# Optimization experiments

Measured on AMD Instinct MI355X. Metric: run time of the kernel, lower is better.

## Reference

```python
import jax, jax.numpy as jnp
import numpy as np

B, SE, HE, DE = 32, 256, 512, 2
HD = DE * HE            # decoder hidden (h0 reshape implies Hd = De*He)
ED = 256                # label embedding dim
N = 8192                # seq label num (output_size)
T = 20                  # decode_max_seq_len (eval path)
KE = VE = 1024
MD = 256
EIN = ED + HE           # LSTM input size
EOS_ID = 0
SPARCE_RATE = 0.8
NEG = -1.0e7
MAXV = 1.0e9
EPS = 1e-8


def setup_inputs() -> dict:
    key = jax.random.key(0)
    ks = jax.random.split(key, 20)
    s = 0.05
    return {
        'encoded_hidden_embeddings': jax.random.normal(ks[0], (B, SE, HE), jnp.float32),
        'hidden': jax.random.normal(ks[1], (DE, B, HE), jnp.float32),
        'cell': jax.random.normal(ks[2], (DE, B, HE), jnp.float32),
        'text_lengths': jax.random.randint(ks[3], (B,), 1, SE + 1),
        'encoder_mask': jnp.ones((B, SE), bool),
        'memory_key_mask': jnp.ones((B, KE), bool),
        'memory_key_embedding': jax.random.normal(ks[4], (B, KE, MD), jnp.float32),
        'memory_value_mask': jnp.ones((B, VE), bool),
        'memory_value_embedding': jax.random.normal(ks[5], (B, VE, MD), jnp.float32),
        # parameters
        'W_ih': jax.random.normal(ks[6], (4 * HD, EIN), jnp.float32) * s,
        'W_hh': jax.random.normal(ks[7], (4 * HD, HD), jnp.float32) * s,
        'b_ih': jnp.zeros((4 * HD,), jnp.float32),
        'b_hh': jnp.zeros((4 * HD,), jnp.float32),
        'mlp_W1': jax.random.normal(ks[8], (HD, HD), jnp.float32) * s,
        'mlp_b1': jnp.zeros((HD,), jnp.float32),
        'mlp_W2': jax.random.normal(ks[9], (N, HD), jnp.float32) * s,
        'mlp_b2': jnp.zeros((N,), jnp.float32),
        'emb_table': jax.random.normal(ks[10], (N, ED), jnp.float32) * s,
        'dense_W': jax.random.normal(ks[11], (HE, ED), jnp.float32) * s,
        'dense_b': jnp.zeros((HE,), jnp.float32),
        'read_W': jax.random.normal(ks[12], (MD, EIN), jnp.float32) * s,
        'read_b': jnp.zeros((MD,), jnp.float32),
    }


def _cos(a, b):
    num = jnp.sum(a * b, axis=-1)
    den = jnp.maximum(jnp.linalg.norm(a, axis=-1) * jnp.linalg.norm(b, axis=-1), EPS)
    return num / den


def _lstm(x, h, c, W_ih, W_hh, b_ih, b_hh):
    g = x @ W_ih.T + b_ih + h @ W_hh.T + b_hh
    i, f, gg, o = jnp.split(g, 4, axis=-1)  # torch gate order i,f,g,o
    c1 = jax.nn.sigmoid(f) * c + jax.nn.sigmoid(i) * jnp.tanh(gg)
    h1 = jax.nn.sigmoid(o) * jnp.tanh(c1)
    return h1, c1


def _forward(enc, hidden, cell, encoder_mask, memory_key_mask, memory_value_mask,
             mem_k, mem_v, W_ih, W_hh, b_ih, b_hh, mlp_W1, mlp_b1, mlp_W2, mlp_b2,
             emb_table, dense_W, dense_b, read_W, read_b):
    h0 = jnp.transpose(hidden, (1, 0, 2)).reshape(B, HD)
    c0 = jnp.transpose(cell, (1, 0, 2)).reshape(B, HD)
    pad = jnp.where(encoder_mask, 0.0, -MAXV).astype(enc.dtype)  # (B,Se)
    sent = enc[:, 0, :]                                           # (B,He)
    x0 = jnp.zeros((B, EIN), enc.dtype)
    mask0 = jnp.zeros((B, N), enc.dtype)

    def step(carry, _):
        h, c, x, lmask = carry
        h, c = _lstm(x, h, c, W_ih, W_hh, b_ih, b_hh)
        hid = jax.nn.relu(h @ mlp_W1.T + mlp_b1)
        logits = hid @ mlp_W2.T + mlp_b2 + lmask          # (B,N)
        nid = jnp.argmax(logits, axis=-1)                 # (B,) greedy decode
        lab = emb_table[nid]                              # (B,Ed)
        lmask = lmask.at[jnp.arange(B), nid].set(NEG)     # scatter-mask used ids
        lmask = lmask.at[:, EOS_ID].set(0.0)              # EOS always allowed
        q = lab @ dense_W.T + dense_b                     # (B,He)
        score = jnp.einsum('bse,be->bs', enc, q) + pad
        w = jax.nn.softmax(score, axis=-1)
        attn = jnp.einsum('bse,bs->be', enc, w)
        x = jnp.concatenate([lab, sent + attn], axis=-1)  # (B,Ed+He)
        mq = x @ read_W.T + read_b                        # (B,Md)
        ksim = _cos(mq[:, None, :], mem_k)                # (B,Ke)
        return (h, c, x, lmask), (logits, nid, ksim)

    _, (outputs, next_ids, key_sims) = jax.lax.scan(step, (h0, c0, x0, mask0), None, length=T)
    outputs = jnp.transpose(outputs, (1, 0, 2))           # (B,T,N)
    next_ids = next_ids.T                                 # (B,T)
    key_sims = jnp.transpose(key_sims, (1, 0, 2))         # (B,T,Ke)

    key_sim = jnp.max(key_sims, axis=1)                   # (B,Ke)
    key_sim = jnp.where(key_sim < 0, 0.0, key_sim)
    # mapping_weight: pairwise cosine between memory keys and values (B,Ke,Ve)
    mw = _cos(mem_k[:, :, None, :], mem_v[:, None, :, :])
    keep = (mw >= jnp.max(mw, axis=-1, keepdims=True)) & (mw >= SPARCE_RATE)
    mw = jnp.where(keep, mw, 0.0)
    val_sim = jnp.einsum('bk,bkv->bv', key_sim, mw)       # (B,Ve)
    key_out = jnp.where(memory_key_mask, key_sim, -1.0)
    val_out = jnp.where(memory_value_mask, val_sim, -1.0)
    return outputs, next_ids, key_out, val_out


def reference(encoded_hidden_embeddings, hidden, cell, text_lengths, encoder_mask,
              memory_key_mask, memory_key_embedding, memory_value_mask, memory_value_embedding,
              W_ih, W_hh, b_ih, b_hh, mlp_W1, mlp_b1, mlp_W2, mlp_b2,
              emb_table, dense_W, dense_b, read_W, read_b):
    del text_lengths  # unused in module math
    return _forward(encoded_hidden_embeddings, hidden, cell, encoder_mask,
                    memory_key_mask, memory_value_mask, memory_key_embedding,
                    memory_value_embedding, W_ih, W_hh, b_ih, b_hh,
                    mlp_W1, mlp_b1, mlp_W2, mlp_b2, emb_table,
                    dense_W, dense_b, read_W, read_b)
```

## Files before the change

kernel.cpp:

```cpp
#include <hip/hip_runtime.h>
#include <cstdint>
#include <cstddef>

#define B_   32
#define SE_  256
#define HE_  512
#define HD_  1024
#define ED_  256
#define N_   8192
#define T_   20
#define KE_  1024
#define VE_  1024
#define MD_  256
#define EIN_ 768
#define NEG_   (-10000000.0f)
#define MAXV_  (1000000000.0f)
#define EPS_   (1e-8f)
#define SPARSE_ 0.8f
#define GATE_  0.78f

#define NLOGB (N_/16)

#define O_IDS  (B_*T_*N_)
#define O_KEY  (O_IDS + B_*T_)
#define O_VAL  (O_KEY + B_*KE_)

typedef __attribute__((ext_vector_type(8))) short short8;
typedef __attribute__((ext_vector_type(4))) float floatx4;

__device__ __forceinline__ float sigf(float v) { return 1.0f / (1.0f + expf(-v)); }

__device__ __forceinline__ short f2bf(float f) {
    union { float f; unsigned u; } v; v.f = f;
    unsigned r = v.u + 0x7FFFu + ((v.u >> 16) & 1u);
    return (short)(r >> 16);
// ... 122 lines not shown
                int byt = (vrow * 512 + kc * 64 + lq * 16) ^ ((vrow & 7) << 4);
                bfr[kc] = *(const short8*)((char*)Vs + byt);
            }
            #pragma unroll
            for (int rg = 0; rg < 2; ++rg) {
                floatx4 acc = {0.0f, 0.0f, 0.0f, 0.0f};
                #pragma unroll
                for (int kc = 0; kc < 8; ++kc)
                    acc = __builtin_amdgcn_mfma_f32_16x16x32_bf16(af[rg][kc], bfr[kc], acc, 0, 0, 0);
                #pragma unroll
                for (int reg = 0; reg < 4; ++reg) {
                    float cs = acc[reg] / fmaxf(nk[rg][reg] * nv, EPS_);
                    rmax[rg][reg] = fmaxf(rmax[rg][reg], cs);
                }
            }
        }
    }
    #pragma unroll
    for (int rg = 0; rg < 2; ++rg)
        #pragma unroll
        for (int reg = 0; reg < 4; ++reg) {
            float v = rmax[rg][reg];
            v = fmaxf(v, __shfl_xor(v, 1, 64));
            v = fmaxf(v, __shfl_xor(v, 2, 64));
            v = fmaxf(v, __shfl_xor(v, 4, 64));
            v = fmaxf(v, __shfl_xor(v, 8, 64));
            if (lrow == 0) {
                int* p = (int*)&rowmax[(size_t)b * KE_ + rowbase + rg * 16 + lq * 4 + reg];
                atomicMax(p, __float_as_int(fmaxf(v, 0.0f)));
            }
        }
}


__global__ __launch_bounds__(256) void k_gates(
    const float* __restrict__ x, const float* __restrict__ W_ih,
    const float* __restrict__ h_in, const float* __restrict__ W_hh,
    const float* __restrict__ b_ih, const float* __restrict__ b_hh,
    float* __restrict__ c_st, float* __restrict__ h_out)
{
    __shared__ __align__(16) float Xs[32 * 256];
    __shared__ float red[16][32][17];
    const int tid = threadIdx.x;
    const int kg = tid & 15, jg = (tid >> 4) & 3, bg = tid >> 6;
    const int ch0 = blockIdx.x * 4;

    float acc[4][8];
    #pragma unroll
    for (int jv = 0; jv < 4; ++jv)
        #pragma unroll
        for (int bv = 0; bv < 8; ++bv) acc[jv][bv] = 0.0f;

    for (int k0 = 0; k0 < EIN_ + HD_; k0 += 256) {
        const bool second = (k0 >= EIN_);
        const float* Xsrc = second ? h_in : x;
        const float* Wsrc = second ? W_hh : W_ih;
        const int srcK = second ? HD_ : EIN_;
        const int ks = second ? (k0 - EIN_) : k0;
        __syncthreads();
        #pragma unroll
        for (int i = 0; i < 8; ++i) {
            int lin = tid + i * 256;
            int bb = lin >> 6, q = lin & 63;
            *(float4*)&Xs[bb * 256 + q * 4] = *(const float4*)(Xsrc + (size_t)bb * srcK + ks + q * 4);
        }
        __syncthreads();
// ... 79 lines not shown
            for (int bv = 0; bv < 8; ++bv) {
                float4 x4 = *(const float4*)&Xs[(bg * 8 + bv) * 256 + qc * 4];
                #pragma unroll
                for (int jv = 0; jv < 4; ++jv) {
                    acc[jv][bv] = fmaf(wv[jv].x, x4.x, acc[jv][bv]);
                    acc[jv][bv] = fmaf(wv[jv].y, x4.y, acc[jv][bv]);
                    acc[jv][bv] = fmaf(wv[jv].z, x4.z, acc[jv][bv]);
                    acc[jv][bv] = fmaf(wv[jv].w, x4.w, acc[jv][bv]);
                }
            }
        }
    }
    #pragma unroll
    for (int jv = 0; jv < 4; ++jv)
        #pragma unroll
        for (int bv = 0; bv < 8; ++bv)
            red[jg * 4 + jv][bg * 8 + bv][kg] = acc[jv][bv];
    __syncthreads();
    for (int o = tid; o < 16 * B_; o += 256) {
        int jjo = o >> 5, b = o & 31;
        float s = 0.0f;
        #pragma unroll
        for (int k = 0; k < 16; ++k) s += red[jjo][b][k];
        int jo = jbase + jjo;
        s += bias[jo];
        if (relu) s = fmaxf(s, 0.0f);
        out[(size_t)b * outStride + jo] = s;
    }
}

__global__ __launch_bounds__(256) void k_logits(
    const float* __restrict__ hid, const float* __restrict__ W2,
    const float* __restrict__ b2, const float* __restrict__ lmask,
    float* __restrict__ lg_out ,
    float* __restrict__ pval, int* __restrict__ pidx)
{
    __shared__ __align__(16) float Xs[32 * 256];
    __shared__ float red[16][32][17];
    const int tid = threadIdx.x;
    const int kg = tid & 15, jg = (tid >> 4) & 3, bg = tid >> 6;
    const int jbase = blockIdx.x * 16;

    float acc[4][8];
    #pragma unroll
    for (int jv = 0; jv < 4; ++jv)
        #pragma unroll
        for (int bv = 0; bv < 8; ++bv) acc[jv][bv] = 0.0f;

    for (int k0 = 0; k0 < HD_; k0 += 256) {
        __syncthreads();
        #pragma unroll
        for (int i = 0; i < 8; ++i) {
            int lin = tid + i * 256;
            int bb = lin >> 6, q = lin & 63;
            *(float4*)&Xs[bb * 256 + q * 4] = *(const float4*)(hid + (size_t)bb * HD_ + k0 + q * 4);
        }
        __syncthreads();
        #pragma unroll
        for (int qq = 0; qq < 4; ++qq) {
            const int qc = kg + qq * 16;
            float4 wv[4];
            #pragma unroll
            for (int jv = 0; jv < 4; ++jv)
                wv[jv] = *(const float4*)(W2 + (size_t)(jbase + jg * 4 + jv) * HD_ + k0 + qc * 4);
            #pragma unroll
            for (int bv = 0; bv < 8; ++bv) {
                float4 x4 = *(const float4*)&Xs[(bg * 8 + bv) * 256 + qc * 4];
                #pragma unroll
// ... 6 lines not shown
            }
        }
    }
    #pragma unroll
    for (int jv = 0; jv < 4; ++jv)
        #pragma unroll
        for (int bv = 0; bv < 8; ++bv)
            red[jg * 4 + jv][bg * 8 + bv][kg] = acc[jv][bv];
    __syncthreads();
    for (int o = tid; o < 16 * B_; o += 256) {
        int jjo = o >> 5, b = o & 31;
        float s = 0.0f;
        #pragma unroll
        for (int k = 0; k < 16; ++k) s += red[jjo][b][k];
        int jo = jbase + jjo;
        s += b2[jo] + lmask[(size_t)b * N_ + jo];
        lg_out[(size_t)b * (T_ * N_) + jo] = s;
        red[jjo][b][16] = s;
    }
    __syncthreads();
    if (tid < 32) {
        int b = tid;
        float best = -1e38f; int bi = 0;
        #pragma unroll
        for (int jjo = 0; jjo < 16; ++jjo) {
            float v = red[jjo][b][16];
            if (v > best) { best = v; bi = jjo; }
        }
        pval[(size_t)b * NLOGB + blockIdx.x] = best;
        pidx[(size_t)b * NLOGB + blockIdx.x] = jbase + bi;
    }
}

__global__ __launch_bounds__(256) void k_merge(
    const float* __restrict__ pval, const int* __restrict__ pidx,
    float* __restrict__ d_out, int t, int* __restrict__ nidbuf,
    float* __restrict__ lmask, const float* __restrict__ emb,
    const float* __restrict__ dense_W, const float* __restrict__ dense_b,
    float* __restrict__ qbuf)
{
    __shared__ float sv[256];
    __shared__ int   si[256];
    __shared__ __align__(16) float lab[ED_];
    const int b = blockIdx.x, tid = threadIdx.x;
    float best = -1e38f; int bi = N_;
    for (int p = tid; p < NLOGB; p += 256) {
        float v = pval[(size_t)b * NLOGB + p];
        int   i = pidx[(size_t)b * NLOGB + p];
        if (v > best || (v == best && i < bi)) { best = v; bi = i; }
    }
    sv[tid] = best; si[tid] = bi;
    __syncthreads();
    for (int s = 128; s > 0; s >>= 1) {
        if (tid < s) {
            float v2 = sv[tid + s]; int i2 = si[tid + s];
            if (v2 > sv[tid] || (v2 == sv[tid] && i2 < si[tid])) { sv[tid] = v2; si[tid] = i2; }
        }
        __syncthreads();
    }
    int nid = si[0];
    if (tid == 0) {
        nidbuf[b] = nid;
        d_out[O_IDS + (size_t)b * T_ + t] = (float)nid;
        lmask[(size_t)b * N_ + nid] = NEG_;
        lmask[(size_t)b * N_] = 0.0f;
    }
    lab[tid] = emb[(size_t)nid * ED_ + tid];
    __syncthreads();
    const float4* Lq = (const float4*)lab;
    #pragma unroll
    for (int jj = 0; jj < 2; ++jj) {
        int j = tid + jj * 256;
        const float4* Wq = (const float4*)(dense_W + (size_t)j * ED_);
        float s0 = 0.0f, s1 = 0.0f, s2 = 0.0f, s3 = 0.0f;
        #pragma unroll
        for (int q = 0; q < 64; q += 4) {
            float4 w0 = Wq[q],   x0 = Lq[q];
            float4 w1 = Wq[q+1], x1 = Lq[q+1];
            float4 w2 = Wq[q+2], x2 = Lq[q+2];
            float4 w3 = Wq[q+3], x3 = Lq[q+3];
            s0 = fmaf(w0.x,x0.x,s0); s0 = fmaf(w0.y,x0.y,s0); s0 = fmaf(w0.z,x0.z,s0); s0 = fmaf(w0.w,x0.w,s0);
            s1 = fmaf(w1.x,x1.x,s1); s1 = fmaf(w1.y,x1.y,s1); s1 = fmaf(w1.z,x1.z,s1); s1 = fmaf(w1.w,x1.w,s1);
            s2 = fmaf(w2.x,x2.x,s2); s2 = fmaf(w2.y,x2.y,s2); s2 = fmaf(w2.z,x2.z,s2); s2 = fmaf(w2.w,x2.w,s2);
            s3 = fmaf(w3.x,x3.x,s3); s3 = fmaf(w3.y,x3.y,s3); s3 = fmaf(w3.z,x3.z,s3); s3 = fmaf(w3.w,x3.w,s3);
        }
        qbuf[(size_t)b * HE_ + j] = dense_b[j] + ((s0 + s1) + (s2 + s3));
    }
}

__device__ __forceinline__ float wave_dot(const float* __restrict__ row, const float* vl, int quads)
{
    int lane = threadIdx.x & 63;
    float s = 0.0f;
    for (int q = lane; q < quads; q += 64) {
        float4 a = ((const float4*)row)[q];
        float4 x = ((const float4*)vl)[q];
        s = fmaf(a.x, x.x, s); s = fmaf(a.y, x.y, s);
        s = fmaf(a.z, x.z, s); s = fmaf(a.w, x.w, s);
    }
    for (int m = 32; m; m >>= 1) s += __shfl_xor(s, m, 64);
    return s;
}

__global__ __launch_bounds__(256) void k_attn1(
    const float* __restrict__ qg, const float* __restrict__ enc,
    const float* __restrict__ pad, float* __restrict__ part)
{
    __shared__ __align__(16) float ql[HE_];
    __shared__ float sc_l[32];
    __shared__ float wp_l[32];
    const int b = blockIdx.y, sc = blockIdx.x;
    const int tid = threadIdx.x, lane = tid & 63, w = tid >> 6;
    ql[tid] = qg[(size_t)b * HE_ + tid];
    ql[tid + 256] = qg[(size_t)b * HE_ + tid + 256];
    __syncthreads();

    #pragma unroll
    for (int i = 0; i < 8; ++i) {
        int sl = w + i * 4;
        int s = sc * 32 + sl;
        float v = wave_dot(enc + ((size_t)b * SE_ + s) * HE_, ql, HE_ / 4);
        if (lane == 0) sc_l[sl] = v + pad[b * SE_ + s];
    }
    __syncthreads();

    float m = -1e38f;
    #pragma unroll
    for (int i = 0; i < 32; ++i) m = fmaxf(m, sc_l[i]);
    if (tid < 32) wp_l[tid] = expf(sc_l[tid] - m);
    __syncthreads();
    float esum = 0.0f;
    #pragma unroll
    for (int i = 0; i < 32; ++i) esum += wp_l[i];

    float a0 = 0.0f, a1 = 0.0f;
    for (int i = 0; i < 32; ++i) {
        float wv = wp_l[i];
        const float* er = enc + ((size_t)b * SE_ + sc * 32 + i) * HE_;
        a0 = fmaf(wv, er[tid], a0);
        a1 = fmaf(wv, er[tid + 256], a1);
    }
    float* pb = part + ((size_t)b * 8 + sc) * 516;
    pb[tid] = a0;
    pb[256 + tid] = a1;
    if (tid == 0) { pb[512] = m; pb[513] = esum; }
}

__global__ __launch_bounds__(256) void k_attn2read(
    const float* __restrict__ part, const float* __restrict__ sent,
    const int* __restrict__ nidbuf, const float* __restrict__ emb,
    const float* __restrict__ read_W, const float* __restrict__ read_b,
    float* __restrict__ xg, float* __restrict__ mqg)
{
    __shared__ float ms[8], es[8];
    __shared__ __align__(16) float xl[EIN_];
    const int qv = blockIdx.x, b = blockIdx.y;
    const int tid = threadIdx.x;
    if (tid < 8) {
        ms[tid] = part[((size_t)b * 8 + tid) * 516 + 512];
        es[tid] = part[((size_t)b * 8 + tid) * 516 + 513];
    }
    __syncthreads();
    float m = -1e38f;
    #pragma unroll
    for (int c = 0; c < 8; ++c) m = fmaxf(m, ms[c]);
    float scale[8];
    float denom = 0.0f;
    #pragma unroll
    for (int c = 0; c < 8; ++c) { scale[c] = expf(ms[c] - m); denom += es[c] * scale[c]; }
    float inv = 1.0f / denom;
    float a0 = 0.0f, a1 = 0.0f;
    #pragma unroll
    for (int c = 0; c < 8; ++c) {
        const float* pb = part + ((size_t)b * 8 + c) * 516;
        a0 = fmaf(scale[c], pb[tid], a0);
        a1 = fmaf(scale[c], pb[256 + tid], a1);
    }
    a0 *= inv; a1 *= inv;
    int nid = nidbuf[b];
    xl[tid]             = emb[(size_t)nid * ED_ + tid];
    xl[ED_ + tid]       = sent[(size_t)b * HE_ + tid]       + a0;
    xl[ED_ + 256 + tid] = sent[(size_t)b * HE_ + 256 + tid] + a1;
    __syncthreads();
    if (qv == 0) {
        float* xr = xg + (size_t)b * EIN_;
        xr[tid] = xl[tid]; xr[tid + 256] = xl[tid + 256]; xr[tid + 512] = xl[tid + 512];
    }
    const int r = qv * 64 + (tid >> 2), kq = tid & 3;
    const float4* Wq = (const float4*)(read_W + (size_t)r * EIN_ + kq * 192);
    const float4* xq = (const float4*)(xl + kq * 192);
    float s0 = 0.0f, s1 = 0.0f, s2 = 0.0f, s3 = 0.0f;
    #pragma unroll
    for (int q = 0; q < 48; q += 4) {
        float4 w0 = Wq[q],   v0 = xq[q];
        float4 w1 = Wq[q+1], v1 = xq[q+1];
        float4 w2 = Wq[q+2], v2 = xq[q+2];
        float4 w3 = Wq[q+3], v3 = xq[q+3];
        s0 = fmaf(w0.x,v0.x,s0); s0 = fmaf(w0.y,v0.y,s0); s0 = fmaf(w0.z,v0.z,s0); s0 = fmaf(w0.w,v0.w,s0);
        s1 = fmaf(w1.x,v1.x,s1); s1 = fmaf(w1.y,v1.y,s1); s1 = fmaf(w1.z,v1.z,s1); s1 = fmaf(w1.w,v1.w,s1);
        s2 = fmaf(w2.x,v2.x,s2); s2 = fmaf(w2.y,v2.y,s2); s2 = fmaf(w2.z,v2.z,s2); s2 = fmaf(w2.w,v2.w,s2);
        s3 = fmaf(w3.x,v3.x,s3); s3 = fmaf(w3.y,v3.y,s3); s3 = fmaf(w3.w,v3.w,s3); s3 = fmaf(w3.z,v3.z,s3);
    }
    float s = ((s0 + s1) + (s2 + s3));
    s += __shfl_xor(s, 1, 64);
    s += __shfl_xor(s, 2, 64);
    if (kq == 0) mqg[(size_t)b * MD_ + r] = s + read_b[r];
}

__global__ __launch_bounds__(256) void k_ksim(
    const float* __restrict__ mqg,
    const float* __restrict__ mem_k, const float* __restrict__ normk,
    float* __restrict__ key_run)
{
    __shared__ __align__(16) float mql[MD_];
    __shared__ float red[256];
    const int b = blockIdx.y, kt = blockIdx.x;
    const int tid = threadIdx.x, lane = tid & 63, w = tid >> 6;
    float mv = mqg[(size_t)b * MD_ + tid];
    mql[tid] = mv;
    red[tid] = mv * mv;
    __syncthreads();
    for (int s = 128; s > 0; s >>= 1) { if (tid < s) red[tid] += red[tid + s]; __syncthreads(); }
    float nmq = sqrtf(red[0]);

    int base = kt * 64 + w * 16;
    for (int i = 0; i < 16; ++i) {
        int k = base + i;
        float num = wave_dot(mem_k + ((size_t)b * KE_ + k) * MD_, mql, MD_ / 4);
        if (lane == 0) {
            float cs = num / fmaxf(nmq * normk[b * KE_ + k], EPS_);
            float o = key_run[b * KE_ + k];
            key_run[b * KE_ + k] = fmaxf(o, cs);
        }
    }
}

__global__ __launch_bounds__(256) void k_keyfinal(
    float* __restrict__ key_run, const void* __restrict__ kmask, float* __restrict__ d_out)
{
    int idx = blockIdx.x * 256 + threadIdx.x;
    bool b8 = mask_is_b8(kmask);
    float v = key_run[idx];
    v = (v < 0.0f) ? 0.0f : v;
    key_run[idx] = v;
    d_out[O_KEY + idx] = mask_at(kmask, idx, b8) ? v : -1.0f;
}

__global__ __launch_bounds__(256) void k_val(
    const float* __restrict__ rowmax, const float* __restrict__ mem_k, const float* __restrict__ mem_v,
    const float* __restrict__ normk, const float* __restrict__ normv,
    const float* __restrict__ key_sim, float* __restrict__ val_sim)
{
    int idx = blockIdx.x * 256 + threadIdx.x;
// ... 40 lines not shown
    const float* mem_k    = (const float*)d_in[6];
    const void*  vmask    = d_in[7];
    const float* mem_v    = (const float*)d_in[8];
    const float* W_ih     = (const float*)d_in[9];
    const float* W_hh     = (const float*)d_in[10];
    const float* b_ih     = (const float*)d_in[11];
    const float* b_hh     = (const float*)d_in[12];
    const float* mlp_W1   = (const float*)d_in[13];
    const float* mlp_b1   = (const float*)d_in[14];
    const float* mlp_W2   = (const float*)d_in[15];
    const float* mlp_b2   = (const float*)d_in[16];
    const float* emb      = (const float*)d_in[17];
    const float* dense_W  = (const float*)d_in[18];
    const float* dense_b  = (const float*)d_in[19];
    const float* read_W   = (const float*)d_in[20];
    const float* read_b   = (const float*)d_in[21];
    float* d_out = (float*)d_out_v;
    float* ws = (float*)d_ws;

    float* hA      = ws;
    float* hB      = ws + 32768;
    float* c       = ws + 65536;
    float* x       = ws + 98304;
    float* hid     = ws + 122880;
    float* lmask   = ws + 155648;
    float* sent    = ws + 417792;
    float* pad     = ws + 434176;
    float* key_run = ws + 442368;
    float* val_sim = ws + 475136;
    float* normk   = ws + 507904;
    float* normv   = ws + 540672;
    float* rowmax  = ws + 573440;
    int*   nidbuf  = (int*)(ws + 606208);
    float* mqg     = ws + 606272;
    float* qbuf    = ws + 614464;
    float* part    = ws + 630848;
    float* pval    = ws + 762944;
    int*   pidx    = (int*)(ws + 779328);

    k_init<<<1024, 256, 0, stream>>>(hidden, cell, enc, encmask, hA, c, x, lmask, sent, pad, key_run, val_sim, rowmax);
    k_norms<<<256, 256, 0, stream>>>(mem_k, mem_v, normk, normv);
    k_rowmax_mfma<<<dim3(8, 4, 32), 256, 0, stream>>>(mem_k, mem_v, normk, normv, rowmax);

    const float* hin = hA;
    float* hout = hB;
    for (int t = 0; t < T_; ++t) {
        k_gates<<<256, 256, 0, stream>>>(x, W_ih, hin, W_hh, b_ih, b_hh, c, hout);
        k_gemm3<<<HD_ / 16, 256, 0, stream>>>(hout, mlp_W1, HD_, mlp_b1, hid, HD_, 1);
        k_logits<<<N_ / 16, 256, 0, stream>>>(hid, mlp_W2, mlp_b2, lmask,
                                              d_out + (size_t)t * N_, pval, pidx);
        k_merge<<<B_, 256, 0, stream>>>(pval, pidx, d_out, t, nidbuf, lmask,
                                        emb, dense_W, dense_b, qbuf);
        k_attn1<<<dim3(8, B_), 256, 0, stream>>>(qbuf, enc, pad, part);
        k_attn2read<<<dim3(4, B_), 256, 0, stream>>>(part, sent, nidbuf, emb, read_W, read_b, x, mqg);
        k_ksim<<<dim3(16, B_), 256, 0, stream>>>(mqg, mem_k, normk, key_run);
        float* tmp = (float*)hin; hin = hout; hout = tmp;
    }

    k_keyfinal<<<128, 256, 0, stream>>>(key_run, kmask, d_out);
    k_val<<<128, 256, 0, stream>>>(rowmax, mem_k, mem_v, normk, normv, key_run, val_sim);
    k_valout<<<128, 256, 0, stream>>>(val_sim, vmask, d_out);
}
```

Measured before the change: 2.900 ms.

## Fuse per-step decoder kernels into one cooperative persistent kernel with grid syncs

Replaces the seven per-timestep kernel launches (140 total) with a single cooperative kernel that loops over timesteps and separates the stages with grid.sync(). The goal is to remove launch overhead and inter-kernel gaps in a latency-bound decode loop. Work per stage is spread over the grid with block-stride loops. The grid is capped at 512 blocks, so the gates and logits stages run with less parallelism than before, and grid-wide barriers carry their own cost. If the cooperative launch is unavailable, the code falls back to the old launch sequence.

```diff
diff --git a/kernel.cpp b/kernel.cpp
--- a/kernel.cpp
+++ b/kernel.cpp
@@ -1,6 +1,9 @@
 #include <hip/hip_runtime.h>
+#include <hip/hip_cooperative_groups.h>
 #include <cstdint>
 #include <cstddef>
+
+namespace cg = cooperative_groups;
 
 #define B_   32
 #define SE_  256
@@ -189,6 +192,397 @@
         }
 }
 
+__device__ __forceinline__ float wave_dot(const float* __restrict__ row, const float* vl, int quads)
+{
+    int lane = threadIdx.x & 63;
+    float s = 0.0f;
+    for (int q = lane; q < quads; q += 64) {
+        float4 a = ((const float4*)row)[q];
+        float4 x = ((const float4*)vl)[q];
+        s = fmaf(a.x, x.x, s); s = fmaf(a.y, x.y, s);
+        s = fmaf(a.z, x.z, s); s = fmaf(a.w, x.w, s);
+    }
+    for (int m = 32; m; m >>= 1) s += __shfl_xor(s, m, 64);
+    return s;
+}
+
+struct MegaArgs {
+    const float *enc, *pad, *sent;
+    const float *W_ih, *W_hh, *b_ih, *b_hh;
+    const float *mlp_W1, *mlp_b1, *mlp_W2, *mlp_b2;
+    const float *emb, *dense_W, *dense_b, *read_W, *read_b;
+    const float *mem_k, *normk;
+    float *hA, *hB, *c, *x, *hid, *lmask, *key_run, *d_out;
+    float *qbuf, *mqg, *part, *pval;
+    int *nidbuf, *pidx;
+};
+
+template<int JV>
+__device__ __forceinline__ void gemm_core(
+    const float* __restrict__ X, int K, const float* __restrict__ W, int jbase,
+    float* Xs, float (*g_red)[33], int tid)
+{
+    const int kg = tid & 15, jg = (tid >> 4) & 3, bg = tid >> 6;
+    float acc[JV][8];
+    #pragma unroll
+    for (int jv = 0; jv < JV; ++jv)
+        #pragma unroll
+        for (int bv = 0; bv < 8; ++bv) acc[jv][bv] = 0.0f;
+
+    for (int k0 = 0; k0 < K; k0 += 256) {
+        __syncthreads();
+        #pragma unroll
+        for (int i = 0; i < 8; ++i) {
+            int lin = tid + i * 256;
+            int bb = lin >> 6, q = lin & 63;
+            *(float4*)&Xs[bb * 256 + q * 4] = *(const float4*)(X + (size_t)bb * K + k0 + q * 4);
+        }
+        __syncthreads();
+        #pragma unroll
+        for (int qq = 0; qq < 4; ++qq) {
+            const int qc = kg + qq * 16;
+            float4 wv[JV];
+            #pragma unroll
+            for (int jv = 0; jv < JV; ++jv)
+                wv[jv] = *(const float4*)(W + (size_t)(jbase + jg * JV + jv) * K + k0 + qc * 4);
+            #pragma unroll
+            for (int bv = 0; bv < 8; ++bv) {
+                float4 x4 = *(const float4*)&Xs[(bg * 8 + bv) * 256 + qc * 4];
+                #pragma unroll
+                for (int jv = 0; jv < JV; ++jv) {
+                    acc[jv][bv] = fmaf(wv[jv].x, x4.x, acc[jv][bv]);
+                    acc[jv][bv] = fmaf(wv[jv].y, x4.y, acc[jv][bv]);
+                    acc[jv][bv] = fmaf(wv[jv].z, x4.z, acc[jv][bv]);
+                    acc[jv][bv] = fmaf(wv[jv].w, x4.w, acc[jv][bv]);
+                }
+            }
+        }
+    }
+    #pragma unroll
+    for (int jv = 0; jv < JV; ++jv)
+        #pragma unroll
+        for (int bv = 0; bv < 8; ++bv) {
+            float v = acc[jv][bv];
+            v += __shfl_xor(v, 1, 64);
+            v += __shfl_xor(v, 2, 64);
+            v += __shfl_xor(v, 4, 64);
+            v += __shfl_xor(v, 8, 64);
+            acc[jv][bv] = v;
+        }
+    __syncthreads();
+    if (kg == 0) {
+        #pragma unroll
+        for (int jv = 0; jv < JV; ++jv)
+            #pragma unroll
+            for (int bv = 0; bv < 8; ++bv)
+                g_red[jg * JV + jv][bg * 8 + bv] = acc[jv][bv];
+    }
+    __syncthreads();
+}
+
+__global__ __launch_bounds__(256) void k_megaloop(MegaArgs a)
+{
+    cg::grid_group grid = cg::this_grid();
+    __shared__ __align__(16) float Xs[32 * 256];
+    __shared__ float g_red[16][33];
+    const int tid = threadIdx.x, lane = tid & 63, w = tid >> 6;
+
+    for (int t = 0; t < T_; ++t) {
+        const float* hin  = (t & 1) ? a.hB : a.hA;
+        float*       hout = (t & 1) ? a.hA : a.hB;
+
+        for (int u = blockIdx.x; u < 512; u += gridDim.x) {
+            const int kg = tid & 15, jg = (tid >> 4) & 3, bg = tid >> 6;
+            const int ch0 = u * 2;
+            float acc[2][8];
+            #pragma unroll
+            for (int jv = 0; jv < 2; ++jv)
+                #pragma unroll
+                for (int bv = 0; bv < 8; ++bv) acc[jv][bv] = 0.0f;
+
+            for (int k0 = 0; k0 < EIN_ + HD_; k0 += 256) {
+                const bool second = (k0 >= EIN_);
+                const float* Xsrc = second ? hin : a.x;
+                const float* Wsrc = second ? a.W_hh : a.W_ih;
+                const int srcK = second ? HD_ : EIN_;
+                const int ks = second ? (k0 - EIN_) : k0;
+                __syncthreads();
+                #pragma unroll
+                for (int i = 0; i < 8; ++i) {
+                    int lin = tid + i * 256;
+                    int bb = lin >> 6, q = lin & 63;
+                    *(float4*)&Xs[bb * 256 + q * 4] = *(const float4*)(Xsrc + (size_t)bb * srcK + ks + q * 4);
+                }
+                __syncthreads();
+                #pragma unroll
+                for (int qq = 0; qq < 4; ++qq) {
+                    const int qc = kg + qq * 16;
+                    float4 wv[2];
+                    #pragma unroll
+                    for (int jv = 0; jv < 2; ++jv)
+                        wv[jv] = *(const float4*)(Wsrc + (size_t)(jg * HD_ + ch0 + jv) * srcK + ks + qc * 4);
+                    #pragma unroll
+                    for (int bv = 0; bv < 8; ++bv) {
+                        float4 x4 = *(const float4*)&Xs[(bg * 8 + bv) * 256 + qc * 4];
+                        #pragma unroll
+                        for (int jv = 0; jv < 2; ++jv) {
+                            acc[jv][bv] = fmaf(wv[jv].x, x4.x, acc[jv][bv]);
+                            acc[jv][bv] = fmaf(wv[jv].y, x4.y, acc[jv][bv]);
+                            acc[jv][bv] = fmaf(wv[jv].z, x4.z, acc[jv][bv]);
+                            acc[jv][bv] = fmaf(wv[jv].w, x4.w, acc[jv][bv]);
+                        }
+                    }
+                }
+            }
+            #pragma unroll
+            for (int jv = 0; jv < 2; ++jv)
+                #pragma unroll
+                for (int bv = 0; bv < 8; ++bv) {
+                    float v = acc[jv][bv];
+                    v += __shfl_xor(v, 1, 64);
+                    v += __shfl_xor(v, 2, 64);
+                    v += __shfl_xor(v, 4, 64);
+                    v += __shfl_xor(v, 8, 64);
+                    acc[jv][bv] = v;
+                }
+            __syncthreads();
+            if (kg == 0) {
+                #pragma unroll
+                for (int jv = 0; jv < 2; ++jv)
+                    #pragma unroll
+                    for (int bv = 0; bv < 8; ++bv)
+                        g_red[jg * 2 + jv][bg * 8 + bv] = acc[jv][bv];
+            }
+            __syncthreads();
+            if (tid < 64) {
+                const int c2 = tid >> 5, b = tid & 31;
+                float g4[4];
+                #pragma unroll
+                for (int gate = 0; gate < 4; ++gate) {
+                    int row = gate * HD_ + ch0 + c2;
+                    g4[gate] = g_red[gate * 2 + c2][b] + a.b_ih[row] + a.b_hh[row];
+                }
+                int idx = b * HD_ + ch0 + c2;
+                float c1 = sigf(g4[1]) * a.c[idx] + sigf(g4[0]) * tanhf(g4[2]);
+                hout[idx] = sigf(g4[3]) * tanhf(c1);
+                a.c[idx] = c1;
+            }
+        }
+        grid.sync();
+
+        for (int u = blockIdx.x; u < 256; u += gridDim.x) {
+            gemm_core<1>(hout, HD_, a.mlp_W1, u * 4, Xs, g_red, tid);
+            if (tid < 128) {
+                int jjo = tid >> 5, b = tid & 31;
+                int jo = u * 4 + jjo;
+                a.hid[(size_t)b * HD_ + jo] = fmaxf(g_red[jjo][b] + a.mlp_b1[jo], 0.0f);
+            }
+        }
+        grid.sync();
+
+        for (int u = blockIdx.x; u < 512; u += gridDim.x) {
+            gemm_core<4>(a.hid, HD_, a.mlp_W2, u * 16, Xs, g_red, tid);
+            for (int o = tid; o < 512; o += 256) {
+                int jjo = o >> 5, b = o & 31;
+                int jo = u * 16 + jjo;
+                float s = g_red[jjo][b] + a.mlp_b2[jo] + a.lmask[(size_t)b * N_ + jo];
+                a.d_out[(size_t)b * (T_ * N_) + (size_t)t * N_ + jo] = s;
+                g_red[jjo][b] = s;
+            }
+            __syncthreads();
+            if (tid < 32) {
+                int b = tid;
+                float best = -1e38f; int bi = 0;
+                #pragma unroll
+                for (int jjo = 0; jjo < 16; ++jjo) {
+                    float v = g_red[jjo][b];
+                    if (v > best) { best = v; bi = jjo; }
+                }
+                a.pval[(size_t)b * NLOGB + u] = best;
+                a.pidx[(size_t)b * NLOGB + u] = u * 16 + bi;
+            }
+            __syncthreads();
+        }
+        grid.sync();
+
+        for (int u = blockIdx.x; u < 32; u += gridDim.x) {
+            const int b = u;
+            float* sv = Xs;
+            int*   si = (int*)(Xs + 256);
+            float* lab = Xs + 512;
+            __syncthreads();
+            float best = -1e38f; int bi = N_;
+            for (int p = tid; p < NLOGB; p += 256) {
+                float v = a.pval[(size_t)b * NLOGB + p];
+                int   i = a.pidx[(size_t)b * NLOGB + p];
+                if (v > best || (v == best && i < bi)) { best = v; bi = i; }
+            }
+            sv[tid] = best; si[tid] = bi;
+            __syncthreads();
+            for (int s = 128; s > 0; s >>= 1) {
+                if (tid < s) {
+                    float v2 = sv[tid + s]; int i2 = si[tid + s];
+                    if (v2 > sv[tid] || (v2 == sv[tid] && i2 < si[tid])) { sv[tid] = v2; si[tid] = i2; }
+                }
+                __syncthreads();
+            }
+            int nid = si[0];
+            if (tid == 0) {
+                a.nidbuf[b] = nid;
+                a.d_out[O_IDS + (size_t)b * T_ + t] = (float)nid;
+                a.lmask[(size_t)b * N_ + nid] = NEG_;
+                a.lmask[(size_t)b * N_] = 0.0f;
+            }
+            lab[tid] = a.emb[(size_t)nid * ED_ + tid];
+            __syncthreads();
+            const float4* Lq = (const float4*)lab;
+            #pragma unroll
+            for (int jj = 0; jj < 2; ++jj) {
+                int j = tid + jj * 256;
+                const float4* Wq = (const float4*)(a.dense_W + (size_t)j * ED_);
+                float s0 = 0.0f, s1 = 0.0f, s2 = 0.0f, s3 = 0.0f;
+                #pragma unroll
+                for (int q = 0; q < 64; q += 4) {
+                    float4 w0 = Wq[q],   x0 = Lq[q];
+                    float4 w1 = Wq[q+1], x1 = Lq[q+1];
+                    float4 w2 = Wq[q+2], x2 = Lq[q+2];
+                    float4 w3 = Wq[q+3], x3 = Lq[q+3];
+                    s0 = fmaf(w0.x,x0.x,s0); s0 = fmaf(w0.y,x0.y,s0); s0 = fmaf(w0.z,x0.z,s0); s0 = fmaf(w0.w,x0.w,s0);
+                    s1 = fmaf(w1.x,x1.x,s1); s1 = fmaf(w1.y,x1.y,s1); s1 = fmaf(w1.z,x1.z,s1); s1 = fmaf(w1.w,x1.w,s1);
+                    s2 = fmaf(w2.x,x2.x,s2); s2 = fmaf(w2.y,x2.y,s2); s2 = fmaf(w2.z,x2.z,s2); s2 = fmaf(w2.w,x2.w,s2);
+                    s3 = fmaf(w3.x,x3.x,s3); s3 = fmaf(w3.y,x3.y,s3); s3 = fmaf(w3.z,x3.z,s3); s3 = fmaf(w3.w,x3.w,s3);
+                }
+                a.qbuf[(size_t)b * HE_ + j] = a.dense_b[j] + ((s0 + s1) + (s2 + s3));
+            }
+            __syncthreads();
+        }
+        grid.sync();
+
+        for (int u = blockIdx.x; u < 256; u += gridDim.x) {
+            const int sc = u & 7, b = u >> 3;
+            float* ql = Xs;
+            float* sc_l = Xs + 512;
+            float* wp_l = Xs + 544;
+            __syncthreads();
+            ql[tid] = a.qbuf[(size_t)b * HE_ + tid];
+            ql[tid + 256] = a.qbuf[(size_t)b * HE_ + tid + 256];
+            __syncthreads();
+            #pragma unroll
+            for (int i = 0; i < 8; ++i) {
+                int sl = w + i * 4;
+                int s = sc * 32 + sl;
+                float v = wave_dot(a.enc + ((size_t)b * SE_ + s) * HE_, ql, HE_ / 4);
+                if (lane == 0) sc_l[sl] = v + a.pad[b * SE_ + s];
+            }
+            __syncthreads();
+            float m = -1e38f;
+            #pragma unroll
+            for (int i = 0; i < 32; ++i) m = fmaxf(m, sc_l[i]);
+            if (tid < 32) wp_l[tid] = expf(sc_l[tid] - m);
+            __syncthreads();
+            float esum = 0.0f;
+            #pragma unroll
+            for (int i = 0; i < 32; ++i) esum += wp_l[i];
+            float a0 = 0.0f, a1 = 0.0f;
+            for (int i = 0; i < 32; ++i) {
+                float wv = wp_l[i];
+                const float* er = a.enc + ((size_t)b * SE_ + sc * 32 + i) * HE_;
+                a0 = fmaf(wv, er[tid], a0);
+                a1 = fmaf(wv, er[tid + 256], a1);
+            }
+            float* pb = a.part + ((size_t)b * 8 + sc) * 516;
+            pb[tid] = a0;
+            pb[256 + tid] = a1;
+            if (tid == 0) { pb[512] = m; pb[513] = esum; }
+            __syncthreads();
+        }
+        grid.sync();
+
+        for (int u = blockIdx.x; u < 128; u += gridDim.x) {
+            const int qv = u & 3, b = u >> 2;
+            float* xl = Xs;
+            float* ms = Xs + 768;
+            float* es = Xs + 776;
+            __syncthreads();
+            if (tid < 8) {
+                ms[tid] = a.part[((size_t)b * 8 + tid) * 516 + 512];
+                es[tid] = a.part[((size_t)b * 8 + tid) * 516 + 513];
+            }
+            __syncthreads();
+            float m = -1e38f;
+            #pragma unroll
+            for (int c8 = 0; c8 < 8; ++c8) m = fmaxf(m, ms[c8]);
+            float scale[8];
+            float denom = 0.0f;
+            #pragma unroll
+            for (int c8 = 0; c8 < 8; ++c8) { scale[c8] = expf(ms[c8] - m); denom += es[c8] * scale[c8]; }
+            float inv = 1.0f / denom;
+            float a0 = 0.0f, a1 = 0.0f;
+            #pragma unroll
+            for (int c8 = 0; c8 < 8; ++c8) {
+                const float* pb = a.part + ((size_t)b * 8 + c8) * 516;
+                a0 = fmaf(scale[c8], pb[tid], a0);
+                a1 = fmaf(scale[c8], pb[256 + tid], a1);
+            }
+            a0 *= inv; a1 *= inv;
+            int nid = a.nidbuf[b];
+            xl[tid]             = a.emb[(size_t)nid * ED_ + tid];
+            xl[ED_ + tid]       = a.sent[(size_t)b * HE_ + tid]       + a0;
+            xl[ED_ + 256 + tid] = a.sent[(size_t)b * HE_ + 256 + tid] + a1;
+            __syncthreads();
+            if (qv == 0) {
+                float* xr = a.x + (size_t)b * EIN_;
+                xr[tid] = xl[tid]; xr[tid + 256] = xl[tid + 256]; xr[tid + 512] = xl[tid + 512];
+            }
+            const int r = qv * 64 + (tid >> 2), kq = tid & 3;
+            const float4* Wq = (const float4*)(a.read_W + (size_t)r * EIN_ + kq * 192);
+            const float4* xq = (const float4*)(xl + kq * 192);
+            float s0 = 0.0f, s1 = 0.0f, s2 = 0.0f, s3 = 0.0f;
+            #pragma unroll
+            for (int q = 0; q < 48; q += 4) {
+                float4 w0 = Wq[q],   v0 = xq[q];
+                float4 w1 = Wq[q+1], v1 = xq[q+1];
+                float4 w2 = Wq[q+2], v2 = xq[q+2];
+                float4 w3 = Wq[q+3], v3 = xq[q+3];
+                s0 = fmaf(w0.x,v0.x,s0); s0 = fmaf(w0.y,v0.y,s0); s0 = fmaf(w0.z,v0.z,s0); s0 = fmaf(w0.w,v0.w,s0);
+                s1 = fmaf(w1.x,v1.x,s1); s1 = fmaf(w1.y,v1.y,s1); s1 = fmaf(w1.z,v1.z,s1); s1 = fmaf(w1.w,v1.w,s1);
+                s2 = fmaf(w2.x,v2.x,s2); s2 = fmaf(w2.y,v2.y,s2); s2 = fmaf(w2.z,v2.z,s2); s2 = fmaf(w2.w,v2.w,s2);
+                s3 = fmaf(w3.x,v3.x,s3); s3 = fmaf(w3.y,v3.y,s3); s3 = fmaf(w3.z,v3.z,s3); s3 = fmaf(w3.w,v3.w,s3);
+            }
+            float s = ((s0 + s1) + (s2 + s3));
+            s += __shfl_xor(s, 1, 64);
+            s += __shfl_xor(s, 2, 64);
+            if (kq == 0) a.mqg[(size_t)b * MD_ + r] = s + a.read_b[r];
+            __syncthreads();
+        }
+        grid.sync();
+
+        for (int u = blockIdx.x; u < 512; u += gridDim.x) {
+            const int kt = u & 15, b = u >> 4;
+            float* mql = Xs;
+            float* red = Xs + 256;
+            __syncthreads();
+            float mv = a.mqg[(size_t)b * MD_ + tid];
+            mql[tid] = mv;
+            red[tid] = mv * mv;
+            __syncthreads();
+            for (int s = 128; s > 0; s >>= 1) { if (tid < s) red[tid] += red[tid + s]; __syncthreads(); }
+            float nmq = sqrtf(red[0]);
+            int base = kt * 64 + w * 16;
+            for (int i = 0; i < 16; ++i) {
+                int k = base + i;
+                float num = wave_dot(a.mem_k + ((size_t)b * KE_ + k) * MD_, mql, MD_ / 4);
+                if (lane == 0) {
+                    float cs = num / fmaxf(nmq * a.normk[b * KE_ + k], EPS_);
+                    float o = a.key_run[b * KE_ + k];
+                    a.key_run[b * KE_ + k] = fmaxf(o, cs);
+                }
+            }
+            __syncthreads();
+        }
+        grid.sync();
+    }
+}
 
 __global__ __launch_bounds__(256) void k_gates(
     const float* __restrict__ x, const float* __restrict__ W_ih,
@@ -334,8 +728,7 @@
 __global__ __launch_bounds__(256) void k_logits(
     const float* __restrict__ hid, const float* __restrict__ W2,
     const float* __restrict__ b2, const float* __restrict__ lmask,
-    float* __restrict__ lg_out ,
-    float* __restrict__ pval, int* __restrict__ pidx)
+    float* __restrict__ lg_out, float* __restrict__ pval, int* __restrict__ pidx)
 {
     __shared__ __align__(16) float Xs[32 * 256];
     __shared__ float red[16][32][17];
@@ -464,20 +857,6 @@
     }
 }
 
-__device__ __forceinline__ float wave_dot(const float* __restrict__ row, const float* vl, int quads)
-{
-    int lane = threadIdx.x & 63;
-    float s = 0.0f;
-    for (int q = lane; q < quads; q += 64) {
-        float4 a = ((const float4*)row)[q];
-        float4 x = ((const float4*)vl)[q];
-        s = fmaf(a.x, x.x, s); s = fmaf(a.y, x.y, s);
-        s = fmaf(a.z, x.z, s); s = fmaf(a.w, x.w, s);
-    }
-    for (int m = 32; m; m >>= 1) s += __shfl_xor(s, m, 64);
-    return s;
-}
-
 __global__ __launch_bounds__(256) void k_attn1(
     const float* __restrict__ qg, const float* __restrict__ enc,
     const float* __restrict__ pad, float* __restrict__ part)
@@ -575,7 +954,7 @@
         s0 = fmaf(w0.x,v0.x,s0); s0 = fmaf(w0.y,v0.y,s0); s0 = fmaf(w0.z,v0.z,s0); s0 = fmaf(w0.w,v0.w,s0);
         s1 = fmaf(w1.x,v1.x,s1); s1 = fmaf(w1.y,v1.y,s1); s1 = fmaf(w1.z,v1.z,s1); s1 = fmaf(w1.w,v1.w,s1);
         s2 = fmaf(w2.x,v2.x,s2); s2 = fmaf(w2.y,v2.y,s2); s2 = fmaf(w2.z,v2.z,s2); s2 = fmaf(w2.w,v2.w,s2);
-        s3 = fmaf(w3.x,v3.x,s3); s3 = fmaf(w3.y,v3.y,s3); s3 = fmaf(w3.w,v3.w,s3); s3 = fmaf(w3.z,v3.z,s3);
+        s3 = fmaf(w3.x,v3.x,s3); s3 = fmaf(w3.y,v3.y,s3); s3 = fmaf(w3.z,v3.z,s3); s3 = fmaf(w3.w,v3.w,s3);
     }
     float s = ((s0 + s1) + (s2 + s3));
     s += __shfl_xor(s, 1, 64);
@@ -711,19 +1090,49 @@
     k_norms<<<256, 256, 0, stream>>>(mem_k, mem_v, normk, normv);
     k_rowmax_mfma<<<dim3(8, 4, 32), 256, 0, stream>>>(mem_k, mem_v, normk, normv, rowmax);
 
-    const float* hin = hA;
-    float* hout = hB;
-    for (int t = 0; t < T_; ++t) {
-        k_gates<<<256, 256, 0, stream>>>(x, W_ih, hin, W_hh, b_ih, b_hh, c, hout);
-        k_gemm3<<<HD_ / 16, 256, 0, stream>>>(hout, mlp_W1, HD_, mlp_b1, hid, HD_, 1);
-        k_logits<<<N_ / 16, 256, 0, stream>>>(hid, mlp_W2, mlp_b2, lmask,
-                                              d_out + (size_t)t * N_, pval, pidx);
-        k_merge<<<B_, 256, 0, stream>>>(pval, pidx, d_out, t, nidbuf, lmask,
-                                        emb, dense_W, dense_b, qbuf);
-        k_attn1<<<dim3(8, B_), 256, 0, stream>>>(qbuf, enc, pad, part);
-        k_attn2read<<<dim3(4, B_), 256, 0, stream>>>(part, sent, nidbuf, emb, read_W, read_b, x, mqg);
-        k_ksim<<<dim3(16, B_), 256, 0, stream>>>(mqg, mem_k, normk, key_run);
-        float* tmp = (float*)hin; hin = hout; hout = tmp;
+    bool coop = true;
+    int maxb = 0;
+    if (hipOccupancyMaxActiveBlocksPerMultiprocessor(&maxb, k_megaloop, 256, 0) != hipSuccess || maxb < 1)
+        coop = false;
+    int ncu = 0;
+    if (coop) {
+        int dev = 0;
+        hipGetDevice(&dev);
+        if (hipDeviceGetAttribute(&ncu, hipDeviceAttributeMultiprocessorCount, dev) != hipSuccess || ncu < 1)
+            coop = false;
+    }
+    if (coop) {
+        int grid = maxb * ncu;
+        if (grid > 512) grid = 512;
+        MegaArgs ma;
+        ma.enc = enc; ma.pad = pad; ma.sent = sent;
+        ma.W_ih = W_ih; ma.W_hh = W_hh; ma.b_ih = b_ih; ma.b_hh = b_hh;
+        ma.mlp_W1 = mlp_W1; ma.mlp_b1 = mlp_b1; ma.mlp_W2 = mlp_W2; ma.mlp_b2 = mlp_b2;
+        ma.emb = emb; ma.dense_W = dense_W; ma.dense_b = dense_b; ma.read_W = read_W; ma.read_b = read_b;
+        ma.mem_k = mem_k; ma.normk = normk;
+        ma.hA = hA; ma.hB = hB; ma.c = c; ma.x = x; ma.hid = hid;
+        ma.lmask = lmask; ma.key_run = key_run; ma.d_out = d_out;
+        ma.qbuf = qbuf; ma.mqg = mqg; ma.part = part; ma.pval = pval;
+        ma.nidbuf = nidbuf; ma.pidx = pidx;
+        void* args[] = { (void*)&ma };
+        hipError_t le = hipLaunchCooperativeKernel(k_megaloop, dim3(grid), dim3(256), args, 0, stream);
+        if (le != hipSuccess) { (void)hipGetLastError(); coop = false; }
+    }
+    if (!coop) {
+        const float* hin = hA;
+        float* hout = hB;
+        for (int t = 0; t < T_; ++t) {
+            k_gates<<<256, 256, 0, stream>>>(x, W_ih, hin, W_hh, b_ih, b_hh, c, hout);
+            k_gemm3<<<HD_ / 16, 256, 0, stream>>>(hout, mlp_W1, HD_, mlp_b1, hid, HD_, 1);
+            k_logits<<<N_ / 16, 256, 0, stream>>>(hid, mlp_W2, mlp_b2, lmask,
+                                                  d_out + (size_t)t * N_, pval, pidx);
+            k_merge<<<B_, 256, 0, stream>>>(pval, pidx, d_out, t, nidbuf, lmask,
+                                            emb, dense_W, dense_b, qbuf);
+            k_attn1<<<dim3(8, B_), 256, 0, stream>>>(qbuf, enc, pad, part);
+            k_attn2read<<<dim3(4, B_), 256, 0, stream>>>(part, sent, nidbuf, emb, read_W, read_b, x, mqg);
+            k_ksim<<<dim3(16, B_), 256, 0, stream>>>(mqg, mem_k, normk, key_run);
+            float* tmp = (float*)hin; hin = hout; hout = tmp;
+        }
     }
 
     k_keyfinal<<<128, 256, 0, stream>>>(key_run, kmask, d_out);
```

Result: no change. 2.903 ms (+0.1%).

## Fuse merge into attention-score kernel and read projection into key-similarity kernel

Applied to the files above, without the earlier changes.

Each decode step drops from seven launches to five. The argmax merge and label dense projection are recomputed redundantly in every attention chunk block, and the memory-read projection is recomputed in every key-similarity tile block. This removes two launches per step and the qbuf and mqg global round trips. In exchange it duplicates the pval reduction and dense_W work eight times and the read_W GEMV sixteen times per batch row.

```diff
diff --git a/kernel.cpp b/kernel.cpp
--- a/kernel.cpp
+++ b/kernel.cpp
@@ -189,6 +189,19 @@
         }
 }
 
+__device__ __forceinline__ float wave_dot(const float* __restrict__ row, const float* vl, int quads)
+{
+    int lane = threadIdx.x & 63;
+    float s = 0.0f;
+    for (int q = lane; q < quads; q += 64) {
+        float4 a = ((const float4*)row)[q];
+        float4 x = ((const float4*)vl)[q];
+        s = fmaf(a.x, x.x, s); s = fmaf(a.y, x.y, s);
+        s = fmaf(a.z, x.z, s); s = fmaf(a.w, x.w, s);
+    }
+    for (int m = 32; m; m >>= 1) s += __shfl_xor(s, m, 64);
+    return s;
+}
 
 __global__ __launch_bounds__(256) void k_gates(
     const float* __restrict__ x, const float* __restrict__ W_ih,
@@ -334,8 +347,7 @@
 __global__ __launch_bounds__(256) void k_logits(
     const float* __restrict__ hid, const float* __restrict__ W2,
     const float* __restrict__ b2, const float* __restrict__ lmask,
-    float* __restrict__ lg_out ,
-    float* __restrict__ pval, int* __restrict__ pidx)
+    float* __restrict__ lg_out, float* __restrict__ pval, int* __restrict__ pidx)
 {
     __shared__ __align__(16) float Xs[32 * 256];
     __shared__ float red[16][32][17];
@@ -408,17 +420,23 @@
     }
 }
 
-__global__ __launch_bounds__(256) void k_merge(
+__global__ __launch_bounds__(256) void k_attn1m(
     const float* __restrict__ pval, const int* __restrict__ pidx,
+    const float* __restrict__ emb, const float* __restrict__ dense_W,
+    const float* __restrict__ dense_b,
+    const float* __restrict__ enc, const float* __restrict__ pad,
     float* __restrict__ d_out, int t, int* __restrict__ nidbuf,
-    float* __restrict__ lmask, const float* __restrict__ emb,
-    const float* __restrict__ dense_W, const float* __restrict__ dense_b,
-    float* __restrict__ qbuf)
+    float* __restrict__ lmask, float* __restrict__ part)
 {
     __shared__ float sv[256];
     __shared__ int   si[256];
     __shared__ __align__(16) float lab[ED_];
-    const int b = blockIdx.x, tid = threadIdx.x;
+    __shared__ __align__(16) float ql[HE_];
+    __shared__ float sc_l[32];
+    __shared__ float wp_l[32];
+    const int b = blockIdx.y, sc = blockIdx.x;
+    const int tid = threadIdx.x, lane = tid & 63, w = tid >> 6;
+
     float best = -1e38f; int bi = N_;
     for (int p = tid; p < NLOGB; p += 256) {
         float v = pval[(size_t)b * NLOGB + p];
@@ -435,7 +453,7 @@
         __syncthreads();
     }
     int nid = si[0];
-    if (tid == 0) {
+    if (sc == 0 && tid == 0) {
         nidbuf[b] = nid;
         d_out[O_IDS + (size_t)b * T_ + t] = (float)nid;
         lmask[(size_t)b * N_ + nid] = NEG_;
@@ -443,6 +461,7 @@
     }
     lab[tid] = emb[(size_t)nid * ED_ + tid];
     __syncthreads();
+
     const float4* Lq = (const float4*)lab;
     #pragma unroll
     for (int jj = 0; jj < 2; ++jj) {
@@ -460,35 +479,8 @@
             s2 = fmaf(w2.x,x2.x,s2); s2 = fmaf(w2.y,x2.y,s2); s2 = fmaf(w2.z,x2.z,s2); s2 = fmaf(w2.w,x2.w,s2);
             s3 = fmaf(w3.x,x3.x,s3); s3 = fmaf(w3.y,x3.y,s3); s3 = fmaf(w3.z,x3.z,s3); s3 = fmaf(w3.w,x3.w,s3);
         }
-        qbuf[(size_t)b * HE_ + j] = dense_b[j] + ((s0 + s1) + (s2 + s3));
-    }
-}
-
-__device__ __forceinline__ float wave_dot(const float* __restrict__ row, const float* vl, int quads)
-{
-    int lane = threadIdx.x & 63;
-    float s = 0.0f;
-    for (int q = lane; q < quads; q += 64) {
-        float4 a = ((const float4*)row)[q];
-        float4 x = ((const float4*)vl)[q];
-        s = fmaf(a.x, x.x, s); s = fmaf(a.y, x.y, s);
-        s = fmaf(a.z, x.z, s); s = fmaf(a.w, x.w, s);
-    }
-    for (int m = 32; m; m >>= 1) s += __shfl_xor(s, m, 64);
-    return s;
-}
-
-__global__ __launch_bounds__(256) void k_attn1(
-    const float* __restrict__ qg, const float* __restrict__ enc,
-    const float* __restrict__ pad, float* __restrict__ part)
-{
-    __shared__ __align__(16) float ql[HE_];
-    __shared__ float sc_l[32];
-    __shared__ float wp_l[32];
-    const int b = blockIdx.y, sc = blockIdx.x;
-    const int tid = threadIdx.x, lane = tid & 63, w = tid >> 6;
-    ql[tid] = qg[(size_t)b * HE_ + tid];
-    ql[tid + 256] = qg[(size_t)b * HE_ + tid + 256];
+        ql[j] = dense_b[j] + ((s0 + s1) + (s2 + s3));
+    }
     __syncthreads();
 
     #pragma unroll
@@ -522,16 +514,20 @@
     if (tid == 0) { pb[512] = m; pb[513] = esum; }
 }
 
-__global__ __launch_bounds__(256) void k_attn2read(
+__global__ __launch_bounds__(256) void k_attn2ksim(
     const float* __restrict__ part, const float* __restrict__ sent,
     const int* __restrict__ nidbuf, const float* __restrict__ emb,
     const float* __restrict__ read_W, const float* __restrict__ read_b,
-    float* __restrict__ xg, float* __restrict__ mqg)
+    const float* __restrict__ mem_k, const float* __restrict__ normk,
+    float* __restrict__ xg, float* __restrict__ key_run)
 {
     __shared__ float ms[8], es[8];
     __shared__ __align__(16) float xl[EIN_];
-    const int qv = blockIdx.x, b = blockIdx.y;
-    const int tid = threadIdx.x;
+    __shared__ __align__(16) float mql[MD_];
+    __shared__ float red[256];
+    const int kt = blockIdx.x, b = blockIdx.y;
+    const int tid = threadIdx.x, lane = tid & 63, w = tid >> 6;
+
     if (tid < 8) {
         ms[tid] = part[((size_t)b * 8 + tid) * 516 + 512];
         es[tid] = part[((size_t)b * 8 + tid) * 516 + 513];
@@ -539,18 +535,18 @@
     __syncthreads();
     float m = -1e38f;
     #pragma unroll
-    for (int c = 0; c < 8; ++c) m = fmaxf(m, ms[c]);
+    for (int c8 = 0; c8 < 8; ++c8) m = fmaxf(m, ms[c8]);
     float scale[8];
     float denom = 0.0f;
     #pragma unroll
-    for (int c = 0; c < 8; ++c) { scale[c] = expf(ms[c] - m); denom += es[c] * scale[c]; }
+    for (int c8 = 0; c8 < 8; ++c8) { scale[c8] = expf(ms[c8] - m); denom += es[c8] * scale[c8]; }
     float inv = 1.0f / denom;
     float a0 = 0.0f, a1 = 0.0f;
     #pragma unroll
-    for (int c = 0; c < 8; ++c) {
-        const float* pb = part + ((size_t)b * 8 + c) * 516;
-        a0 = fmaf(scale[c], pb[tid], a0);
-        a1 = fmaf(scale[c], pb[256 + tid], a1);
+    for (int c8 = 0; c8 < 8; ++c8) {
+        const float* pb = part + ((size_t)b * 8 + c8) * 516;
+        a0 = fmaf(scale[c8], pb[tid], a0);
+        a1 = fmaf(scale[c8], pb[256 + tid], a1);
     }
     a0 *= inv; a1 *= inv;
     int nid = nidbuf[b];
@@ -558,43 +554,30 @@
     xl[ED_ + tid]       = sent[(size_t)b * HE_ + tid]       + a0;
     xl[ED_ + 256 + tid] = sent[(size_t)b * HE_ + 256 + tid] + a1;
     __syncthreads();
-    if (qv == 0) {
+    if (kt == 0) {
         float* xr = xg + (size_t)b * EIN_;
         xr[tid] = xl[tid]; xr[tid + 256] = xl[tid + 256]; xr[tid + 512] = xl[tid + 512];
     }
-    const int r = qv * 64 + (tid >> 2), kq = tid & 3;
-    const float4* Wq = (const float4*)(read_W + (size_t)r * EIN_ + kq * 192);
-    const float4* xq = (const float4*)(xl + kq * 192);
-    float s0 = 0.0f, s1 = 0.0f, s2 = 0.0f, s3 = 0.0f;
-    #pragma unroll
-    for (int q = 0; q < 48; q += 4) {
-        float4 w0 = Wq[q],   v0 = xq[q];
-        float4 w1 = Wq[q+1], v1 = xq[q+1];
-        float4 w2 = Wq[q+2], v2 = xq[q+2];
-        float4 w3 = Wq[q+3], v3 = xq[q+3];
-        s0 = fmaf(w0.x,v0.x,s0); s0 = fmaf(w0.y,v0.y,s0); s0 = fmaf(w0.z,v0.z,s0); s0 = fmaf(w0.w,v0.w,s0);
-        s1 = fmaf(w1.x,v1.x,s1); s1 = fmaf(w1.y,v1.y,s1); s1 = fmaf(w1.z,v1.z,s1); s1 = fmaf(w1.w,v1.w,s1);
-        s2 = fmaf(w2.x,v2.x,s2); s2 = fmaf(w2.y,v2.y,s2); s2 = fmaf(w2.z,v2.z,s2); s2 = fmaf(w2.w,v2.w,s2);
-        s3 = fmaf(w3.x,v3.x,s3); s3 = fmaf(w3.y,v3.y,s3); s3 = fmaf(w3.w,v3.w,s3); s3 = fmaf(w3.z,v3.z,s3);
-    }
-    float s = ((s0 + s1) + (s2 + s3));
-    s += __shfl_xor(s, 1, 64);
-    s += __shfl_xor(s, 2, 64);
-    if (kq == 0) mqg[(size_t)b * MD_ + r] = s + read_b[r];
-}
-
-__global__ __launch_bounds__(256) void k_ksim(
-    const float* __restrict__ mqg,
-    const float* __restrict__ mem_k, const float* __restrict__ normk,
-    float* __restrict__ key_run)
-{
-    __shared__ __align__(16) float mql[MD_];
-    __shared__ float red[256];
-    const int b = blockIdx.y, kt = blockIdx.x;
-    const int tid = threadIdx.x, lane = tid & 63, w = tid >> 6;
-    float mv = mqg[(size_t)b * MD_ + tid];
-    mql[tid] = mv;
-    red[tid] = mv * mv;
+
+    {
+        const float4* Wq = (const float4*)(read_W + (size_t)tid * EIN_);
+        const float4* xq = (const float4*)xl;
+        float s0 = 0.0f, s1 = 0.0f, s2 = 0.0f, s3 = 0.0f;
+        #pragma unroll
+        for (int q = 0; q < 192; q += 4) {
+            float4 w0 = Wq[q],   v0 = xq[q];
+            float4 w1 = Wq[q+1], v1 = xq[q+1];
+            float4 w2 = Wq[q+2], v2 = xq[q+2];
+            float4 w3 = Wq[q+3], v3 = xq[q+3];
+            s0 = fmaf(w0.x,v0.x,s0); s0 = fmaf(w0.y,v0.y,s0); s0 = fmaf(w0.z,v0.z,s0); s0 = fmaf(w0.w,v0.w,s0);
+            s1 = fmaf(w1.x,v1.x,s1); s1 = fmaf(w1.y,v1.y,s1); s1 = fmaf(w1.z,v1.z,s1); s1 = fmaf(w1.w,v1.w,s1);
+            s2 = fmaf(w2.x,v2.x,s2); s2 = fmaf(w2.y,v2.y,s2); s2 = fmaf(w2.z,v2.z,s2); s2 = fmaf(w2.w,v2.w,s2);
+            s3 = fmaf(w3.x,v3.x,s3); s3 = fmaf(w3.y,v3.y,s3); s3 = fmaf(w3.z,v3.z,s3); s3 = fmaf(w3.w,v3.w,s3);
+        }
+        float mv = read_b[tid] + ((s0 + s1) + (s2 + s3));
+        mql[tid] = mv;
+        red[tid] = mv * mv;
+    }
     __syncthreads();
     for (int s = 128; s > 0; s >>= 1) { if (tid < s) red[tid] += red[tid + s]; __syncthreads(); }
     float nmq = sqrtf(red[0]);
@@ -701,8 +684,6 @@
     float* normv   = ws + 540672;
     float* rowmax  = ws + 573440;
     int*   nidbuf  = (int*)(ws + 606208);
-    float* mqg     = ws + 606272;
-    float* qbuf    = ws + 614464;
     float* part    = ws + 630848;
     float* pval    = ws + 762944;
     int*   pidx    = (int*)(ws + 779328);
@@ -718,11 +699,10 @@
         k_gemm3<<<HD_ / 16, 256, 0, stream>>>(hout, mlp_W1, HD_, mlp_b1, hid, HD_, 1);
         k_logits<<<N_ / 16, 256, 0, stream>>>(hid, mlp_W2, mlp_b2, lmask,
                                               d_out + (size_t)t * N_, pval, pidx);
-        k_merge<<<B_, 256, 0, stream>>>(pval, pidx, d_out, t, nidbuf, lmask,
-                                        emb, dense_W, dense_b, qbuf);
-        k_attn1<<<dim3(8, B_), 256, 0, stream>>>(qbuf, enc, pad, part);
-        k_attn2read<<<dim3(4, B_), 256, 0, stream>>>(part, sent, nidbuf, emb, read_W, read_b, x, mqg);
-        k_ksim<<<dim3(16, B_), 256, 0, stream>>>(mqg, mem_k, normk, key_run);
+        k_attn1m<<<dim3(8, B_), 256, 0, stream>>>(pval, pidx, emb, dense_W, dense_b,
+                                                  enc, pad, d_out, t, nidbuf, lmask, part);
+        k_attn2ksim<<<dim3(16, B_), 256, 0, stream>>>(part, sent, nidbuf, emb, read_W, read_b,
+                                                      mem_k, normk, x, key_run);
         float* tmp = (float*)hin; hin = hout; hout = tmp;
     }
 
```

Measured after the change: 3.737 ms. 1.29x slower.
